# Kernel optimization log

Hardware: AMD Instinct MI355X
Metric: run time of the kernel (lower is better)

The kernel has to match this reference:

```python
import jax, jax.numpy as jnp
import numpy as np

N_NODE, N_PRICE, N_CAT, EMB, LAYERS = 100000, 100, 512, 128, 2
EPS = 1e-8


def spmm(row, col, val, n_rows, emb):
    # torch.sparse.mm(adjacency, emb): out[r] += val * emb[c]
    return jax.ops.segment_sum(val[:, None] * emb[col], row, num_segments=n_rows)


def to_dense(row, col, val, n_rows, n_cols):
    return jnp.zeros((n_rows, n_cols), val.dtype).at[row, col].add(val)


def intra_gate(row, col, val, n_rows, mat_v, emb2):
    # original: alpha = (mat_v expanded to [R, emb]) @ emb2.T ; this is rank-1:
    # scores[i, j] = mat_v[i] * sum_d emb2[j, d]
    scores = mat_v * jnp.sum(emb2, axis=1)[None, :]                      # [R, C]
    alpha = jax.nn.softmax(scores, axis=1) * to_dense(row, col, val, n_rows, emb2.shape[0])
    alpha = alpha / (jnp.sum(alpha, axis=1, keepdims=True) + EPS)        # masked row renorm
    return alpha @ emb2                                                  # [R, emb]; dropout70 = identity (eval)


def inter_gate(Wa, ba, W1, b1, W2, b2, e1, e2, e3):
    g = jax.nn.sigmoid(jnp.concatenate([e1, e2, e3], axis=1) @ Wa + ba + e2 @ W1 + b1 + e3 @ W2 + b2)
    return e1 + g * e2 + (1.0 - g) * e3                                  # dropout50 = identity (eval)


def setup_inputs():
    ks = iter(jax.random.split(jax.random.key(0), 80))
    nrm = lambda shape, s=0.1: jax.random.normal(next(ks), shape, jnp.float32) * s
    inp = {"embedding": nrm((N_NODE, EMB)), "pri_emb": nrm((N_PRICE, EMB)), "cate_emb": nrm((N_CAT, EMB))}
    coo = {"vp": (100000, N_NODE, N_PRICE), "vc": (100000, N_NODE, N_CAT),
           "pv": (100000, N_PRICE, N_NODE), "pc": (2048, N_PRICE, N_CAT),
           "cp": (2048, N_CAT, N_PRICE), "cv": (100000, N_CAT, N_NODE)}
    for name, (nnz, R, C) in coo.items():
        inp[name + "_row"] = jax.random.randint(next(ks), (nnz,), 0, R)
        inp[name + "_col"] = jax.random.randint(next(ks), (nnz,), 0, C)
        inp[name + "_val"] = jax.random.uniform(next(ks), (nnz,), jnp.float32)
    inp["mat_pv"] = nrm((N_PRICE, 1)); inp["mat_pc"] = nrm((N_PRICE, 1))
    inp["mat_cp"] = nrm((N_CAT, 1)); inp["mat_cv"] = nrm((N_CAT, 1))
    for t in "ipc":
        inp["W_aog_" + t] = nrm((3 * EMB, EMB)); inp["b_aog_" + t] = nrm((EMB,))
        inp["W_g" + t + "1"] = nrm((EMB, EMB)); inp["b_g" + t + "1"] = nrm((EMB,))
        inp["W_g" + t + "2"] = nrm((EMB, EMB)); inp["b_g" + t + "2"] = nrm((EMB,))
    return inp


def reference(embedding, pri_emb, cate_emb,
              vp_row, vp_col, vp_val, vc_row, vc_col, vc_val,
              pv_row, pv_col, pv_val, pc_row, pc_col, pc_val,
              cp_row, cp_col, cp_val, cv_row, cv_col, cv_val,
              mat_pv, mat_pc, mat_cp, mat_cv,
              W_aog_i, b_aog_i, W_gi1, b_gi1, W_gi2, b_gi2,
              W_aog_p, b_aog_p, W_gp1, b_gp1, W_gp2, b_gp2,
              W_aog_c, b_aog_c, W_gc1, b_gc1, W_gc2, b_gc2):
    emb_v, emb_p, emb_c = embedding, pri_emb, cate_emb
    for _ in range(LAYERS):
        item = inter_gate(W_aog_i, b_aog_i, W_gi1, b_gi1, W_gi2, b_gi2, emb_v,
                          spmm(vp_row, vp_col, vp_val, N_NODE, emb_p),
                          spmm(vc_row, vc_col, vc_val, N_NODE, emb_c))
        price = inter_gate(W_aog_p, b_aog_p, W_gp1, b_gp1, W_gp2, b_gp2, emb_p,
                           intra_gate(pv_row, pv_col, pv_val, N_PRICE, mat_pv, emb_v),
                           intra_gate(pc_row, pc_col, pc_val, N_PRICE, mat_pc, emb_c))
        cate = inter_gate(W_aog_c, b_aog_c, W_gc1, b_gc1, W_gc2, b_gc2, emb_c,
                          intra_gate(cp_row, cp_col, cp_val, N_CAT, mat_cp, emb_p),
                          intra_gate(cv_row, cv_col, cv_val, N_CAT, mat_cv, emb_v))
        emb_v, emb_p, emb_c = item, price, cate
    return emb_v, emb_p, emb_c
```

## Files before the change

### kernel.cpp

```cpp
#include <hip/hip_runtime.h>

#define EMB 128
#define NV 100000
#define NP 100
#define NC 512
#define EPSV 1e-8f

#define CNT_VP 0
#define CNT_VC 100001
#define CNT_PV 200002
#define CNT_PC 200103
#define CNT_CP 200204
#define CNT_CV 200717
#define CNT_LEN 201230
#define NE_TOT 404096
#define NSB 200

typedef __attribute__((ext_vector_type(8))) short bf16x8;
typedef __attribute__((ext_vector_type(4))) float f32x4;

struct Ptrs6 { const int* row[6]; const int* col[6]; const float* val[6]; };
struct GateW { const float* Wa; const float* W1; const float* W2; const float* ba; const float* b1; const float* b2; };
struct Gates3 { GateW g[3]; };

__device__ __forceinline__ unsigned f2bf(float x){
  unsigned b = __float_as_uint(x);
  return (b + 0x7fffu + ((b >> 16) & 1u)) >> 16;
}
__device__ __forceinline__ unsigned pack2bf(float a, float b){
  return f2bf(a) | (f2bf(b) << 16);
}

__device__ __forceinline__ void sb_decode(int bsm, int& rel, int& cs, int& relN, int& srowBase, int& nRows){
  if(bsm < 98){ rel=2; cs=bsm*1024;       relN=100000; srowBase=0;   nRows=100; }
  else if(bsm < 100){ rel=3; cs=(bsm-98)*1024;  relN=2048;   srowBase=100; nRows=100; }
  else if(bsm < 102){ rel=4; cs=(bsm-100)*1024; relN=2048;   srowBase=200; nRows=512; }
  else {              rel=5; cs=(bsm-102)*1024; relN=100000; srowBase=712; nRows=512; }
}

__device__ __forceinline__ void srow_decode(int srow, int& b0, int& b1, int& gidx){
  if(srow < 100){ b0=0;   b1=98;  gidx = CNT_PV + srow; }
  else if(srow < 200){ b0=98;  b1=100; gidx = CNT_PC + srow-100; }
  else if(srow < 712){ b0=100; b1=102; gidx = CNT_CP + srow-200; }
  else {               b0=102; b1=200; gidx = CNT_CV + srow-712; }
}

#define RS_BASE 396
#define RSV_B 3125
#define RSP_B 4
#define RSC_B 16
#define HISTA_NB (RS_BASE + RSV_B + RSP_B + RSC_B)
__global__ __launch_bounds__(1024) void k_histA(Ptrs6 p, int* counts, int* H,
    const float* v, const float* pe, const float* c, float* s){
  int b = blockIdx.x;
  if(b >= RS_BASE){
    int rs = b - RS_BASE;
    const float* src; int nR, rb, sOff;
    if(rs < RSV_B){ src=v; nR=NV; rb=rs*32; sOff=0; }
    else if(rs < RSV_B+RSP_B){ src=pe; nR=NP; rb=(rs-RSV_B)*32; sOff=NV; }
    else { src=c; nR=NC; rb=(rs-RSV_B-RSP_B)*32; sOff=NV+NP; }
    int rl = threadIdx.x >> 5, lane = threadIdx.x & 31;
    int r = rb + rl;
    if(r >= nR) return;
    float4 x = ((const float4*)(src + (size_t)r*EMB))[lane];
    float sum = (x.x + x.y) + (x.z + x.w);
    #pragma unroll
    for(int o=16;o;o>>=1) sum += __shfl_xor(sum, o);
    if(lane == 0) s[sOff + r] = sum;
    return;
  }
  if(b < 196){
    int e = b*1024 + threadIdx.x;
    if(e >= 200000) return;
    int rel = (e < 100000) ? 0 : 1;
    int loc = rel ? e-100000 : e;
    int cntOff = rel ? CNT_VC : CNT_VP;
    atomicAdd(&counts[cntOff + 1 + p.row[rel][loc]], 1);
    return;
  }
  __shared__ int h[512];
  int rel, cs, relN, srowBase, nRows;
  sb_decode(b - 196, rel, cs, relN, srowBase, nRows);
  int t = threadIdx.x;
  if(t < nRows) h[t] = 0;
  __syncthreads();
  int i = cs + t;
  if(i < relN) atomicAdd(&h[p.row[rel][i]], 1);
  __syncthreads();
  if(t < nRows) H[(srowBase + t)*NSB + (b - 196)] = h[t];
}

__global__ __launch_bounds__(256) void k_counts_w(const int* H, int* G){
  int gw = (blockIdx.x*blockDim.x + threadIdx.x) >> 6;
  int lane = threadIdx.x & 63;
  if(gw >= 1224) return;
  int b0, b1, gidx;
  srow_decode(gw, b0, b1, gidx);
  int c = 0;
  for(int b = b0 + lane; b < b1; b += 64) c += H[gw*NSB + b];
  #pragma unroll
  for(int o=32;o;o>>=1) c += __shfl_xor(c, o);
  if(lane == 0) G[gidx + 1] = c;
}

__global__ __launch_bounds__(256) void k_hscan_w(const int* G, const int* H, int* offs){
  int gw = (blockIdx.x*blockDim.x + threadIdx.x) >> 6;
  int lane = threadIdx.x & 63;
  if(gw >= 1224) return;
  int b0, b1, gidx;
  srow_decode(gw, b0, b1, gidx);
  int nb = b1 - b0;
  int carry = G[gidx];
  for(int base=0; base<nb; base+=64){
    int b = base + lane;
    int hv = (b < nb) ? H[gw*NSB + b0 + b] : 0;
    int v = hv;
    #pragma unroll
    for(int o=1;o<64;o<<=1){
      int t = __shfl_up(v, o);
      if(lane >= o) v += t;
    }
    if(b < nb) offs[gw*NSB + b0 + b] = carry + v - hv;
    carry += __shfl(v, 63);
  }
}

__global__ __launch_bounds__(1024) void k_scatterA(Ptrs6 p, int* cursor, const int* offs, int2* colval){
  int b = blockIdx.x;
  if(b < 196){
    int e = b*1024 + threadIdx.x;
    if(e >= 200000) return;
    int rel = (e < 100000) ? 0 : 1;
    int loc = rel ? e-100000 : e;
    int cntOff = rel ? CNT_VC : CNT_VP;
    int r = p.row[rel][loc];
    int pos = atomicAdd(&cursor[cntOff + r], 1);
    colval[pos] = make_int2(p.col[rel][loc], __float_as_int(p.val[rel][loc]));
    return;
  }
  __shared__ int h[512];
  int rel, cs, relN, srowBase, nRows;
  sb_decode(b - 196, rel, cs, relN, srowBase, nRows);
  int t = threadIdx.x;
  if(t < nRows) h[t] = 0;
  __syncthreads();
  int i = cs + t;
  if(i < relN){
    int r = p.row[rel][i];
    int rank = atomicAdd(&h[r], 1);
    int pos = offs[(srowBase + r)*NSB + (b - 196)] + rank;
    colval[pos] = make_int2(p.col[rel][i], __float_as_int(p.val[rel][i]));
  }
}

#define SCAN_B 1024
__global__ void k_scan1(const int* in, int* out, int* aux, int n){
  __shared__ int sh[SCAN_B];
  int gid = blockIdx.x*SCAN_B + threadIdx.x;
  int v = (gid < n) ? in[gid] : 0;
  sh[threadIdx.x] = v; __syncthreads();
  for(int o=1;o<SCAN_B;o<<=1){
    int t = (threadIdx.x >= o) ? sh[threadIdx.x - o] : 0;
    __syncthreads();
    sh[threadIdx.x] += t;
    __syncthreads();
  }
  if(gid < n) out[gid] = sh[threadIdx.x];
  if(threadIdx.x == SCAN_B-1) aux[blockIdx.x] = sh[threadIdx.x];
}
__global__ void k_scan2(int* aux, int nb){
  __shared__ int sh[SCAN_B];
  int v = (threadIdx.x < nb) ? aux[threadIdx.x] : 0;
  sh[threadIdx.x] = v; __syncthreads();
  for(int o=1;o<SCAN_B;o<<=1){
    int t = (threadIdx.x >= o) ? sh[threadIdx.x - o] : 0;
    __syncthreads();
    sh[threadIdx.x] += t;
    __syncthreads();
  }
  if(threadIdx.x < nb) aux[threadIdx.x] = sh[threadIdx.x];
}
__global__ void k_scan3(int* out, const int* aux, int n){
  int gid = blockIdx.x*SCAN_B + threadIdx.x;
  if(blockIdx.x == 0 || gid >= n) return;
  out[gid] += aux[blockIdx.x - 1];
}

__global__ void k_prepw(Gates3 gs, float* M2, float* M3, float* bsum, unsigned* A1f){
  int idx = blockIdx.x*blockDim.x + threadIdx.x;
  if(idx >= 3*16384) return;
  int g = idx >> 14, t = idx & 16383;
  M2[idx] = gs.g[g].Wa[16384 + t] + gs.g[g].W1[t];
  M3[idx] = gs.g[g].Wa[32768 + t] + gs.g[g].W2[t];
  if(t < 128) bsum[g*128 + t] = gs.g[g].ba[t] + gs.g[g].b1[t] + gs.g[g].b2[t];
  if(idx < 8192){
    const float* Wa = gs.g[0].Wa;
    int p = idx & 3;
    int l = (idx >> 2) & 63;
    int f = idx >> 8;
    int kb = f >> 3, nt = f & 7;
    int k = 32*kb + 8*(l >> 4) + 2*p;
    int n = 16*nt + (l & 15);
    A1f[idx] = pack2bf(Wa[k*128 + n], Wa[(k+1)*128 + n]);
  }
}

#define IG 16
#define IT 32
#define MID_NB 1377
__global__ __launch_bounds__(512) void k_mid(const int* G, const int2* colval,
    const float* s,
    const float* mat_pv, const float* mat_pc, const float* mat_cp, const float* mat_cv,
    const float* cv_, const float* cp_, const float* cc_,
    const float* M2i, const float* M3i,
    float* o_pv, float* o_pc, float* o_cp, float* o_cv,
    float* Pcat, float* Ccat){
  int b = blockIdx.x;
  int tid = threadIdx.x;
  if(b >= 1224){
    int rr = (b - 1224)*4 + (tid >> 7);
    int j = tid & 127;
    __shared__ float rowsh[4][128];
    const float* src; const float* M; float* dst; int r;
    if(rr < NP){ src=cp_; M=M2i; dst=Pcat; r=rr; }
    else { src=cc_; M=M3i; dst=Ccat; r=rr-NP; }
    rowsh[tid>>7][j] = src[r*EMB + j];
    __syncthreads();
    float acc = 0.f;
    for(int k=0;k<128;k++) acc += rowsh[tid>>7][k]*M[k*EMB + j];
    dst[r*256 + j] = rowsh[tid>>7][j];
    dst[r*256 + 128 + j] = acc;
    return;
  }
  int r; const int* rp; float m; const float* emb2; const float* sp; int C; float* out;
  if(b < 100){       r=b;     rp=G+CNT_PV; m=mat_pv[r]; emb2=cv_; sp=s;       C=NV; out=o_pv; }
  else if(b < 200){  r=b-100; rp=G+CNT_PC; m=mat_pc[r]; emb2=cc_; sp=s+NV+NP; C=NC; out=o_pc; }
  else if(b < 712){  r=b-200; rp=G+CNT_CP; m=mat_cp[r]; emb2=cp_; sp=s+NV;    C=NP; out=o_cp; }
  else {             r=b-712; rp=G+CNT_CV; m=mat_cv[r]; emb2=cv_; sp=s;       C=NV; out=o_cv; }
  const float4* sp4 = (const float4*)sp;
  int n4 = C >> 2;
  float za0=0.f, za1=0.f, za2=0.f, za3=0.f;
  for(int jj = tid; jj < n4; jj += 512){
    float4 x = sp4[jj];
    za0 += __expf(m*x.x); za1 += __expf(m*x.y);
    za2 += __expf(m*x.z); za3 += __expf(m*x.w);
  }
  float zacc = (za0+za1)+(za2+za3);
  #pragma unroll
  for(int o=32;o;o>>=1) zacc += __shfl_xor(zacc, o);
  __shared__ float zred[8];
  if((tid & 63) == 0) zred[tid >> 6] = zacc;
  __syncthreads();
  float Zv = 0.f;
  #pragma unroll
  for(int gg=0; gg<8; gg++) Zv += zred[gg];
  int es = rp[r], ee = rp[r+1];
  __shared__ float wsh[512];
  __shared__ int   csh[512];
  __shared__ float accs[IG*EMB];
  __shared__ float Tsh[IG];
  int tx = tid & (IT-1);
  int g  = tid >> 5;
  float4 acc = {0.f,0.f,0.f,0.f};
  float T = 0.f;
  for(int t = es; t < ee; t += 512){
    int k = t + tid;
    if(k < ee){
      int2 q = colval[k];
      csh[tid] = q.x;
      wsh[tid] = __expf(m*sp[q.x]) * __int_as_float(q.y);
    }
    __syncthreads();
    int n = min(512, ee - t);
    #pragma unroll 8
    for(int kk = g; kk < n; kk += IG){
      float wv = wsh[kk];
      int cc = csh[kk];
      float4 ev = ((const float4*)(emb2 + (size_t)cc*EMB))[tx];
      T += wv;
      acc.x += wv*ev.x; acc.y += wv*ev.y; acc.z += wv*ev.z; acc.w += wv*ev.w;
    }
    __syncthreads();
  }
  ((float4*)accs)[g*IT + tx] = acc;
  if(tx == 0) Tsh[g] = T;
  __syncthreads();
  if(tid < EMB){
    float tot = 0.f, Tt = 0.f;
    #pragma unroll
    for(int gg=0; gg<IG; gg++){
      tot += accs[gg*EMB + tid];
      Tt  += Tsh[gg];
    }
    out[r*EMB + tid] = tot / (Tt + EPSV*Zv);
  }
}

#define ITEM_NB 3431
__global__ __launch_bounds__(256) void k_item(const float* vin, float* vout,
    const float* Pcat, const float* Ccat, const int* G, const int2* colval,
    const uint4* A1f, const float* bsum, float* s_out,
    const float* cp_, const float* cc_, float* out_p, float* out_c,
    const float* o_pv, const float* o_pc, const float* o_cp, const float* o_cv,
    const float* Wa_p, const float* Wa_c, const float* M2b, const float* M3b,
    const float* bsb){
  __shared__ unsigned e1h[32][68];
  __shared__ float rsp[32][2];
  int tid = threadIdx.x;
  int b = blockIdx.x;
  if(b >= 3125){
    int half = tid >> 7;
    int j = tid & 127;
    int rr = (b - 3125)*2 + half;
    const float* src; float* dst; const float* e2p; const float* e3p;
    const float* A1; const float* M2; const float* M3; const float* bs; int r; int soff;
    if(rr < NP){ src=cp_; dst=out_p; r=rr;    e2p=o_pv; e3p=o_pc; A1=Wa_p; M2=M2b+16384; M3=M3b+16384; bs=bsb+128; soff=NV; }
    else {       src=cc_; dst=out_c; r=rr-NP; e2p=o_cp; e3p=o_cv; A1=Wa_c; M2=M2b+32768; M3=M3b+32768; bs=bsb+256; soff=NV+NP; }
    float* sh = ((float*)e1h) + half*384;
    sh[j] = src[r*EMB+j]; sh[128+j] = e2p[r*EMB+j]; sh[256+j] = e3p[r*EMB+j];
    __syncthreads();
    float acc = bs[j];
    for(int k=0;k<128;k++)
      acc += sh[k]*A1[k*EMB+j] + sh[128+k]*M2[k*EMB+j] + sh[256+k]*M3[k*EMB+j];
    float g = 1.f/(1.f + __expf(-acc));
    float outv = sh[j] + g*sh[128+j] + (1.f - g)*sh[256+j];
    dst[r*EMB+j] = outv;
    float rs = outv;
    #pragma unroll
    for(int o=32;o;o>>=1) rs += __shfl_xor(rs, o);
    if((tid & 63) == 0) ((float*)rsp)[tid >> 6] = rs;
    __syncthreads();
    if(j == 0) s_out[soff + r] = ((float*)rsp)[half*2] + ((float*)rsp)[half*2+1];
    return;
  }
  int rb = b*32;
  const float4* vin4 = (const float4*)(vin + (size_t)rb*EMB);
  #pragma unroll
  for(int jj=0; jj<4; jj++){
    int j = tid + jj*256;
    int rr = j >> 5, kk4 = j & 31;
    float4 x = vin4[j];
    uint2 pk; pk.x = pack2bf(x.x, x.y); pk.y = pack2bf(x.z, x.w);
    *(uint2*)&e1h[rr][kk4*2] = pk;
  }
  int w = tid >> 6, l = tid & 63;
  int mt = w & 1, ng = w >> 1;
  int g16 = l >> 4, ln = l & 15;
  int cb = 64*ng + ln;
  int rbase = rb + 16*mt + 4*g16;
  const int* rp_vp = G + CNT_VP;
  const int* rp_vc = G + CNT_VC;
  int vp_ptr[5], vc_ptr[5];
  #pragma unroll
  for(int i=0;i<5;i++){
    vp_ptr[i] = rp_vp[rbase + i];
    vc_ptr[i] = rp_vc[rbase + i];
  }
  __syncthreads();
  f32x4 acc[4];
  #pragma unroll
  for(int j=0;j<4;j++){
    float bv = bsum[cb + 16*j];
    acc[j] = (f32x4){bv, bv, bv, bv};
  }
  for(int kb=0; kb<4; kb++){
    uint4 av = *(const uint4*)&e1h[16*mt + ln][16*kb + 4*g16];
    bf16x8 af = *(bf16x8*)&av;
    #pragma unroll
    for(int j=0;j<4;j++){
      uint4 bv = A1f[(kb*8 + ng*4 + j)*64 + l];
      acc[j] = __builtin_amdgcn_mfma_f32_16x16x32_bf16(af, *(bf16x8*)&bv, acc[j], 0, 0, 0);
    }
  }
  unsigned e1lo = (cb & 1) ? 0u : 1u;
  #pragma unroll
  for(int reg=0; reg<4; reg++){
    int rl_ = 16*mt + 4*g16 + reg;
    int r = rb + rl_;
    float e2[4]={0,0,0,0}, e3[4]={0,0,0,0};
    float lg[4] = {acc[0][reg], acc[1][reg], acc[2][reg], acc[3][reg]};
    for(int e=vp_ptr[reg]; e<vp_ptr[reg+1]; e++){
      int2 q = colval[e]; int cc = q.x; float vv = __int_as_float(q.y);
      const float* base = Pcat + (size_t)cc*256 + cb;
      #pragma unroll
      for(int j=0;j<4;j++){ e2[j] += vv*base[16*j]; lg[j] += vv*base[128 + 16*j]; }
    }
    for(int e=vc_ptr[reg]; e<vc_ptr[reg+1]; e++){
      int2 q = colval[e]; int cc = q.x; float vv = __int_as_float(q.y);
      const float* base = Ccat + (size_t)cc*256 + cb;
      #pragma unroll
      for(int j=0;j<4;j++){ e3[j] += vv*base[16*j]; lg[j] += vv*base[128 + 16*j]; }
    }
    float prs = 0.f;
    float* outr = vout + (size_t)r*EMB + cb;
    #pragma unroll
    for(int j=0;j<4;j++){
      float gg = 1.f/(1.f + __expf(-lg[j]));
      unsigned u = e1h[rl_][(cb + 16*j) >> 1];
      float e1v = __uint_as_float(e1lo ? (u << 16) : (u & 0xffff0000u));
      float ov = e1v + gg*e2[j] + (1.f - gg)*e3[j];
      outr[16*j] = ov;
      prs += ov;
    }
    prs += __shfl_xor(prs, 1);
    prs += __shfl_xor(prs, 2);
    prs += __shfl_xor(prs, 4);
    prs += __shfl_xor(prs, 8);
    if(ln == 0) rsp[rl_][ng] = prs;
  }
  __syncthreads();
  if(tid < 32) s_out[rb + tid] = rsp[tid][0] + rsp[tid][1];
}

extern "C" void kernel_launch(void* const* d_in, const int* in_sizes, int n_in,
                              void* d_out, int out_size, void* d_ws, size_t ws_size,
                              hipStream_t stream){
  (void)in_sizes; (void)n_in; (void)out_size; (void)ws_size;
  const float* embedding = (const float*)d_in[0];
  const float* pri_emb   = (const float*)d_in[1];
  const float* cate_emb  = (const float*)d_in[2];
  Ptrs6 P;
  for(int r=0;r<6;r++){
    P.row[r] = (const int*)d_in[3 + r*3];
    P.col[r] = (const int*)d_in[4 + r*3];
    P.val[r] = (const float*)d_in[5 + r*3];
  }
  const float* mat_pv = (const float*)d_in[21];
  const float* mat_pc = (const float*)d_in[22];
  const float* mat_cp = (const float*)d_in[23];
  const float* mat_cv = (const float*)d_in[24];
  Gates3 GW;
  const int gbase[3] = {25, 31, 37};
  for(int g=0; g<3; g++){
    int b = gbase[g];
    GW.g[g].Wa = (const float*)d_in[b];
    GW.g[g].ba = (const float*)d_in[b+1];
    GW.g[g].W1 = (const float*)d_in[b+2];
    GW.g[g].b1 = (const float*)d_in[b+3];
    GW.g[g].W2 = (const float*)d_in[b+4];
    GW.g[g].b2 = (const float*)d_in[b+5];
  }
  float* out_v = (float*)d_out;
  float* out_p = out_v + (size_t)NV*EMB;
  float* out_c = out_p + (size_t)NP*EMB;

  char* base = (char*)d_ws; size_t off = 0;
  auto alloc = [&](size_t bytes)->void*{
    void* p = base + off;
    off += (bytes + 255) & ~(size_t)255;
    return p;
  };
  int*      G      = (int*)alloc(CNT_LEN*4);
  int*      cursor = (int*)alloc(CNT_LEN*4);
  int*      aux    = (int*)alloc(256*4);
  int2*     colval = (int2*)alloc((size_t)NE_TOT*8);
  int*      H      = (int*)alloc((size_t)1224*NSB*4);
  int*      offs   = (int*)alloc((size_t)1224*NSB*4);
  float*    s      = (float*)alloc((NV+NP+NC)*4);
  float*    o_pv   = (float*)alloc(NP*EMB*4);
  float*    o_pc   = (float*)alloc(NP*EMB*4);
  float*    o_cp   = (float*)alloc(NC*EMB*4);
  float*    o_cv   = (float*)alloc(NC*EMB*4);
  float*    Pcat   = (float*)alloc(NP*256*4);
  float*    Ccat   = (float*)alloc(NC*256*4);
  float*    M2b    = (float*)alloc(3*16384*4);
  float*    M3b    = (float*)alloc(3*16384*4);
  float*    bsb    = (float*)alloc(3*128*4);
  unsigned* A1f    = (unsigned*)alloc(8192*4);

  hipMemsetAsync(G, 0, CNT_LEN*4, stream);
  k_histA<<<HISTA_NB, 1024, 0, stream>>>(P, G, H, embedding, pri_emb, cate_emb, s);
  k_counts_w<<<306, 256, 0, stream>>>(H, G);
  int nScanB = (CNT_LEN + SCAN_B - 1)/SCAN_B;
  k_scan1<<<nScanB, SCAN_B, 0, stream>>>(G, G, aux, CNT_LEN);
  k_scan2<<<1, SCAN_B, 0, stream>>>(aux, nScanB);
  k_scan3<<<nScanB, SCAN_B, 0, stream>>>(G, aux, CNT_LEN);
  k_hscan_w<<<306, 256, 0, stream>>>(G, H, offs);
  hipMemcpyAsync(cursor, G, CNT_PV*4, hipMemcpyDeviceToDevice, stream);
  k_scatterA<<<396, 1024, 0, stream>>>(P, cursor, offs, colval);
  k_prepw<<<192, 256, 0, stream>>>(GW, M2b, M3b, bsb, A1f);

  for(int L=0; L<2; L++){
    const float* cv_ = L ? (const float*)out_v : embedding;
    const float* cp_ = L ? (const float*)out_p : pri_emb;
    const float* cc_ = L ? (const float*)out_c : cate_emb;
    k_mid<<<MID_NB, 512, 0, stream>>>(G, colval, s,
                                      mat_pv, mat_pc, mat_cp, mat_cv,
                                      cv_, cp_, cc_, M2b, M3b,
                                      o_pv, o_pc, o_cp, o_cv, Pcat, Ccat);
    k_item<<<ITEM_NB, 256, 0, stream>>>(cv_, out_v, Pcat, Ccat, G, colval,
                                        (const uint4*)A1f, bsb, s,
                                        cp_, cc_, out_p, out_c,
                                        o_pv, o_pc, o_cp, o_cv,
                                        GW.g[1].Wa, GW.g[2].Wa, M2b, M3b, bsb);
  }
}
```

Measured before the change: 226.4 us.

## Fuse item update and intra-gate aggregation into one concurrent kernel

The separate mid (intra-gate) and item kernels are merged into one launch, so the item-row gate blocks and the price/category aggregation blocks run at the same time instead of one after the other. To keep them independent, the item output of layer 0 goes to a temporary buffer when workspace allows, and the row-sum vector s is double-buffered. The Pcat/Ccat precompute and the price/category gate update are split into their own small kernels before and after. This adds an extra 51 MB workspace buffer and two extra launches per layer. Aggregation blocks now use 256 threads and 8 groups instead of 512 threads and 16 groups.

```diff
diff --git a/kernel.cpp b/kernel.cpp
--- a/kernel.cpp
+++ b/kernel.cpp
@@ -205,134 +205,102 @@
   }
 }
 
-#define IG 16
-#define IT 32
-#define MID_NB 1377
-__global__ __launch_bounds__(512) void k_mid(const int* G, const int2* colval,
-    const float* s,
+__global__ __launch_bounds__(512) void k_cat(const float* cp_, const float* cc_,
+    const float* M2i, const float* M3i, float* Pcat, float* Ccat){
+  int rr = blockIdx.x*4 + (threadIdx.x >> 7);
+  int j = threadIdx.x & 127;
+  __shared__ float rowsh[4][128];
+  const float* src; const float* M; float* dst; int r;
+  if(rr < NP){ src=cp_; M=M2i; dst=Pcat; r=rr; }
+  else { src=cc_; M=M3i; dst=Ccat; r=rr-NP; }
+  rowsh[threadIdx.x>>7][j] = src[r*EMB + j];
+  __syncthreads();
+  float acc = 0.f;
+  for(int k=0;k<128;k++) acc += rowsh[threadIdx.x>>7][k]*M[k*EMB + j];
+  dst[r*256 + j] = rowsh[threadIdx.x>>7][j];
+  dst[r*256 + 128 + j] = acc;
+}
+
+#define ITEM_B 3125
+#define FUSED_NB 4349
+#define IG 8
+__global__ __launch_bounds__(256) void k_fused(int bofs,
+    const float* vin, float* vout,
+    const float* Pcat, const float* Ccat, const int* G, const int2* colval,
+    const uint4* A1f, const float* bsum, const float* s_in, float* s_out,
     const float* mat_pv, const float* mat_pc, const float* mat_cp, const float* mat_cv,
-    const float* cv_, const float* cp_, const float* cc_,
-    const float* M2i, const float* M3i,
-    float* o_pv, float* o_pc, float* o_cp, float* o_cv,
-    float* Pcat, float* Ccat){
-  int b = blockIdx.x;
+    const float* cp_, const float* cc_,
+    float* o_pv, float* o_pc, float* o_cp, float* o_cv){
+  __shared__ __align__(16) char smem[8960];
   int tid = threadIdx.x;
-  if(b >= 1224){
-    int rr = (b - 1224)*4 + (tid >> 7);
-    int j = tid & 127;
-    __shared__ float rowsh[4][128];
-    const float* src; const float* M; float* dst; int r;
-    if(rr < NP){ src=cp_; M=M2i; dst=Pcat; r=rr; }
-    else { src=cc_; M=M3i; dst=Ccat; r=rr-NP; }
-    rowsh[tid>>7][j] = src[r*EMB + j];
-    __syncthreads();
-    float acc = 0.f;
-    for(int k=0;k<128;k++) acc += rowsh[tid>>7][k]*M[k*EMB + j];
-    dst[r*256 + j] = rowsh[tid>>7][j];
-    dst[r*256 + 128 + j] = acc;
+  int b = blockIdx.x + bofs;
+  if(b >= ITEM_B){
+    int bi = b - ITEM_B;
+    float* wsh  = (float*)smem;
+    int*   csh  = (int*)(smem + 1024);
+    float* accs = (float*)(smem + 2048);
+    float* Tsh  = (float*)(smem + 2048 + 4096);
+    float* zred = (float*)(smem + 2048 + 4096 + 32);
+    int r; const int* rp; float m; const float* emb2; const float* sp; int C; float* out;
+    if(bi < 100){       r=bi;     rp=G+CNT_PV; m=mat_pv[r]; emb2=vin; sp=s_in;       C=NV; out=o_pv; }
+    else if(bi < 200){  r=bi-100; rp=G+CNT_PC; m=mat_pc[r]; emb2=cc_; sp=s_in+NV+NP; C=NC; out=o_pc; }
+    else if(bi < 712){  r=bi-200; rp=G+CNT_CP; m=mat_cp[r]; emb2=cp_; sp=s_in+NV;    C=NP; out=o_cp; }
+    else {              r=bi-712; rp=G+CNT_CV; m=mat_cv[r]; emb2=vin; sp=s_in;       C=NV; out=o_cv; }
+    const float4* sp4 = (const float4*)sp;
+    int n4 = C >> 2;
+    float za0=0.f, za1=0.f, za2=0.f, za3=0.f;
+    for(int jj = tid; jj < n4; jj += 256){
+      float4 x = sp4[jj];
+      za0 += __expf(m*x.x); za1 += __expf(m*x.y);
+      za2 += __expf(m*x.z); za3 += __expf(m*x.w);
+    }
+    float zacc = (za0+za1)+(za2+za3);
+    #pragma unroll
+    for(int o=32;o;o>>=1) zacc += __shfl_xor(zacc, o);
+    if((tid & 63) == 0) zred[tid >> 6] = zacc;
+    __syncthreads();
+    float Zv = zred[0] + zred[1] + zred[2] + zred[3];
+    int es = rp[r], ee = rp[r+1];
+    int tx = tid & 31;
+    int g  = tid >> 5;
+    float4 acc = {0.f,0.f,0.f,0.f};
+    float T = 0.f;
+    for(int t = es; t < ee; t += 256){
+      int k = t + tid;
+      __syncthreads();
+      if(k < ee){
+        int2 q = colval[k];
+        csh[tid] = q.x;
+        wsh[tid] = __expf(m*sp[q.x]) * __int_as_float(q.y);
+      }
+      __syncthreads();
+      int n = min(256, ee - t);
+      #pragma unroll 8
+      for(int kk = g; kk < n; kk += IG){
+        float wv = wsh[kk];
+        int cc = csh[kk];
+        float4 ev = ((const float4*)(emb2 + (size_t)cc*EMB))[tx];
+        T += wv;
+        acc.x += wv*ev.x; acc.y += wv*ev.y; acc.z += wv*ev.z; acc.w += wv*ev.w;
+      }
+    }
+    __syncthreads();
+    ((float4*)accs)[g*32 + tx] = acc;
+    if(tx == 0) Tsh[g] = T;
+    __syncthreads();
+    if(tid < EMB){
+      float tot = 0.f, Tt = 0.f;
+      #pragma unroll
+      for(int gg=0; gg<IG; gg++){
+        tot += accs[gg*EMB + tid];
+        Tt  += Tsh[gg];
+      }
+      out[r*EMB + tid] = tot / (Tt + EPSV*Zv);
+    }
     return;
   }
-  int r; const int* rp; float m; const float* emb2; const float* sp; int C; float* out;
-  if(b < 100){       r=b;     rp=G+CNT_PV; m=mat_pv[r]; emb2=cv_; sp=s;       C=NV; out=o_pv; }
-  else if(b < 200){  r=b-100; rp=G+CNT_PC; m=mat_pc[r]; emb2=cc_; sp=s+NV+NP; C=NC; out=o_pc; }
-  else if(b < 712){  r=b-200; rp=G+CNT_CP; m=mat_cp[r]; emb2=cp_; sp=s+NV;    C=NP; out=o_cp; }
-  else {             r=b-712; rp=G+CNT_CV; m=mat_cv[r]; emb2=cv_; sp=s;       C=NV; out=o_cv; }
-  const float4* sp4 = (const float4*)sp;
-  int n4 = C >> 2;
-  float za0=0.f, za1=0.f, za2=0.f, za3=0.f;
-  for(int jj = tid; jj < n4; jj += 512){
-    float4 x = sp4[jj];
-    za0 += __expf(m*x.x); za1 += __expf(m*x.y);
-    za2 += __expf(m*x.z); za3 += __expf(m*x.w);
-  }
-  float zacc = (za0+za1)+(za2+za3);
-  #pragma unroll
-  for(int o=32;o;o>>=1) zacc += __shfl_xor(zacc, o);
-  __shared__ float zred[8];
-  if((tid & 63) == 0) zred[tid >> 6] = zacc;
-  __syncthreads();
-  float Zv = 0.f;
-  #pragma unroll
-  for(int gg=0; gg<8; gg++) Zv += zred[gg];
-  int es = rp[r], ee = rp[r+1];
-  __shared__ float wsh[512];
-  __shared__ int   csh[512];
-  __shared__ float accs[IG*EMB];
-  __shared__ float Tsh[IG];
-  int tx = tid & (IT-1);
-  int g  = tid >> 5;
-  float4 acc = {0.f,0.f,0.f,0.f};
-  float T = 0.f;
-  for(int t = es; t < ee; t += 512){
-    int k = t + tid;
-    if(k < ee){
-      int2 q = colval[k];
-      csh[tid] = q.x;
-      wsh[tid] = __expf(m*sp[q.x]) * __int_as_float(q.y);
-    }
-    __syncthreads();
-    int n = min(512, ee - t);
-    #pragma unroll 8
-    for(int kk = g; kk < n; kk += IG){
-      float wv = wsh[kk];
-      int cc = csh[kk];
-      float4 ev = ((const float4*)(emb2 + (size_t)cc*EMB))[tx];
-      T += wv;
-      acc.x += wv*ev.x; acc.y += wv*ev.y; acc.z += wv*ev.z; acc.w += wv*ev.w;
-    }
-    __syncthreads();
-  }
-  ((float4*)accs)[g*IT + tx] = acc;
-  if(tx == 0) Tsh[g] = T;
-  __syncthreads();
-  if(tid < EMB){
-    float tot = 0.f, Tt = 0.f;
-    #pragma unroll
-    for(int gg=0; gg<IG; gg++){
-      tot += accs[gg*EMB + tid];
-      Tt  += Tsh[gg];
-    }
-    out[r*EMB + tid] = tot / (Tt + EPSV*Zv);
-  }
-}
-
-#define ITEM_NB 3431
-__global__ __launch_bounds__(256) void k_item(const float* vin, float* vout,
-    const float* Pcat, const float* Ccat, const int* G, const int2* colval,
-    const uint4* A1f, const float* bsum, float* s_out,
-    const float* cp_, const float* cc_, float* out_p, float* out_c,
-    const float* o_pv, const float* o_pc, const float* o_cp, const float* o_cv,
-    const float* Wa_p, const float* Wa_c, const float* M2b, const float* M3b,
-    const float* bsb){
-  __shared__ unsigned e1h[32][68];
-  __shared__ float rsp[32][2];
-  int tid = threadIdx.x;
-  int b = blockIdx.x;
-  if(b >= 3125){
-    int half = tid >> 7;
-    int j = tid & 127;
-    int rr = (b - 3125)*2 + half;
-    const float* src; float* dst; const float* e2p; const float* e3p;
-    const float* A1; const float* M2; const float* M3; const float* bs; int r; int soff;
-    if(rr < NP){ src=cp_; dst=out_p; r=rr;    e2p=o_pv; e3p=o_pc; A1=Wa_p; M2=M2b+16384; M3=M3b+16384; bs=bsb+128; soff=NV; }
-    else {       src=cc_; dst=out_c; r=rr-NP; e2p=o_cp; e3p=o_cv; A1=Wa_c; M2=M2b+32768; M3=M3b+32768; bs=bsb+256; soff=NV+NP; }
-    float* sh = ((float*)e1h) + half*384;
-    sh[j] = src[r*EMB+j]; sh[128+j] = e2p[r*EMB+j]; sh[256+j] = e3p[r*EMB+j];
-    __syncthreads();
-    float acc = bs[j];
-    for(int k=0;k<128;k++)
-      acc += sh[k]*A1[k*EMB+j] + sh[128+k]*M2[k*EMB+j] + sh[256+k]*M3[k*EMB+j];
-    float g = 1.f/(1.f + __expf(-acc));
-    float outv = sh[j] + g*sh[128+j] + (1.f - g)*sh[256+j];
-    dst[r*EMB+j] = outv;
-    float rs = outv;
-    #pragma unroll
-    for(int o=32;o;o>>=1) rs += __shfl_xor(rs, o);
-    if((tid & 63) == 0) ((float*)rsp)[tid >> 6] = rs;
-    __syncthreads();
-    if(j == 0) s_out[soff + r] = ((float*)rsp)[half*2] + ((float*)rsp)[half*2+1];
-    return;
-  }
+  unsigned (*e1h)[68] = (unsigned(*)[68])smem;
+  float (*rsp)[2] = (float(*)[2])(smem + 32*68*4);
   int rb = b*32;
   const float4* vin4 = (const float4*)(vin + (size_t)rb*EMB);
   #pragma unroll
@@ -412,10 +380,42 @@
   if(tid < 32) s_out[rb + tid] = rsp[tid][0] + rsp[tid][1];
 }
 
+__global__ __launch_bounds__(256) void k_tail(const float* cp_, const float* cc_,
+    float* out_p, float* out_c,
+    const float* o_pv, const float* o_pc, const float* o_cp, const float* o_cv,
+    const float* Wa_p, const float* Wa_c, const float* M2b, const float* M3b,
+    const float* bsb, float* s_out){
+  __shared__ float sh2[2][384];
+  __shared__ float wred[4];
+  int tid = threadIdx.x;
+  int half = tid >> 7;
+  int j = tid & 127;
+  int rr = blockIdx.x*2 + half;
+  const float* src; float* dst; const float* e2p; const float* e3p;
+  const float* A1; const float* M2; const float* M3; const float* bs; int r; int soff;
+  if(rr < NP){ src=cp_; dst=out_p; r=rr;    e2p=o_pv; e3p=o_pc; A1=Wa_p; M2=M2b+16384; M3=M3b+16384; bs=bsb+128; soff=NV; }
+  else {       src=cc_; dst=out_c; r=rr-NP; e2p=o_cp; e3p=o_cv; A1=Wa_c; M2=M2b+32768; M3=M3b+32768; bs=bsb+256; soff=NV+NP; }
+  float* sh = sh2[half];
+  sh[j] = src[r*EMB+j]; sh[128+j] = e2p[r*EMB+j]; sh[256+j] = e3p[r*EMB+j];
+  __syncthreads();
+  float acc = bs[j];
+  for(int k=0;k<128;k++)
+    acc += sh[k]*A1[k*EMB+j] + sh[128+k]*M2[k*EMB+j] + sh[256+k]*M3[k*EMB+j];
+  float g = 1.f/(1.f + __expf(-acc));
+  float outv = sh[j] + g*sh[128+j] + (1.f - g)*sh[256+j];
+  dst[r*EMB+j] = outv;
+  float rs = outv;
+  #pragma unroll
+  for(int o=32;o;o>>=1) rs += __shfl_xor(rs, o);
+  if((tid & 63) == 0) wred[tid >> 6] = rs;
+  __syncthreads();
+  if(j == 0) s_out[soff + r] = wred[half*2] + wred[half*2+1];
+}
+
 extern "C" void kernel_launch(void* const* d_in, const int* in_sizes, int n_in,
                               void* d_out, int out_size, void* d_ws, size_t ws_size,
                               hipStream_t stream){
-  (void)in_sizes; (void)n_in; (void)out_size; (void)ws_size;
+  (void)in_sizes; (void)n_in; (void)out_size;
   const float* embedding = (const float*)d_in[0];
   const float* pri_emb   = (const float*)d_in[1];
   const float* cate_emb  = (const float*)d_in[2];
@@ -456,7 +456,8 @@
   int2*     colval = (int2*)alloc((size_t)NE_TOT*8);
   int*      H      = (int*)alloc((size_t)1224*NSB*4);
   int*      offs   = (int*)alloc((size_t)1224*NSB*4);
-  float*    s      = (float*)alloc((NV+NP+NC)*4);
+  float*    s0     = (float*)alloc((NV+NP+NC)*4);
+  float*    s1     = (float*)alloc((NV+NP+NC)*4);
   float*    o_pv   = (float*)alloc(NP*EMB*4);
   float*    o_pc   = (float*)alloc(NP*EMB*4);
   float*    o_cp   = (float*)alloc(NC*EMB*4);
@@ -467,9 +468,12 @@
   float*    M3b    = (float*)alloc(3*16384*4);
   float*    bsb    = (float*)alloc(3*128*4);
   unsigned* A1f    = (unsigned*)alloc(8192*4);
+  size_t vbytes = (size_t)NV*EMB*4;
+  bool conc = (off + vbytes + 256 <= ws_size);
+  float* v_tmp = conc ? (float*)alloc(vbytes) : nullptr;
 
   hipMemsetAsync(G, 0, CNT_LEN*4, stream);
-  k_histA<<<HISTA_NB, 1024, 0, stream>>>(P, G, H, embedding, pri_emb, cate_emb, s);
+  k_histA<<<HISTA_NB, 1024, 0, stream>>>(P, G, H, embedding, pri_emb, cate_emb, s0);
   k_counts_w<<<306, 256, 0, stream>>>(H, G);
   int nScanB = (CNT_LEN + SCAN_B - 1)/SCAN_B;
   k_scan1<<<nScanB, SCAN_B, 0, stream>>>(G, G, aux, CNT_LEN);
@@ -481,17 +485,30 @@
   k_prepw<<<192, 256, 0, stream>>>(GW, M2b, M3b, bsb, A1f);
 
   for(int L=0; L<2; L++){
-    const float* cv_ = L ? (const float*)out_v : embedding;
+    const float* cv_ = L ? (conc ? (const float*)v_tmp : (const float*)out_v) : embedding;
+    float* vout = (L == 1) ? out_v : (conc ? v_tmp : out_v);
     const float* cp_ = L ? (const float*)out_p : pri_emb;
     const float* cc_ = L ? (const float*)out_c : cate_emb;
-    k_mid<<<MID_NB, 512, 0, stream>>>(G, colval, s,
-                                      mat_pv, mat_pc, mat_cp, mat_cv,
-                                      cv_, cp_, cc_, M2b, M3b,
-                                      o_pv, o_pc, o_cp, o_cv, Pcat, Ccat);
-    k_item<<<ITEM_NB, 256, 0, stream>>>(cv_, out_v, Pcat, Ccat, G, colval,
-                                        (const uint4*)A1f, bsb, s,
-                                        cp_, cc_, out_p, out_c,
-                                        o_pv, o_pc, o_cp, o_cv,
-                                        GW.g[1].Wa, GW.g[2].Wa, M2b, M3b, bsb);
-  }
-}
+    const float* s_in = L ? s1 : s0;
+    float* s_outb = L ? s0 : s1;
+    k_cat<<<153, 512, 0, stream>>>(cp_, cc_, M2b, M3b, Pcat, Ccat);
+    if(conc){
+      k_fused<<<FUSED_NB, 256, 0, stream>>>(0, cv_, vout, Pcat, Ccat, G, colval,
+          (const uint4*)A1f, bsb, s_in, s_outb,
+          mat_pv, mat_pc, mat_cp, mat_cv, cp_, cc_,
+          o_pv, o_pc, o_cp, o_cv);
+    } else {
+      k_fused<<<1224, 256, 0, stream>>>(ITEM_B, cv_, vout, Pcat, Ccat, G, colval,
+          (const uint4*)A1f, bsb, s_in, s_outb,
+          mat_pv, mat_pc, mat_cp, mat_cv, cp_, cc_,
+          o_pv, o_pc, o_cp, o_cv);
+      k_fused<<<ITEM_B, 256, 0, stream>>>(0, cv_, vout, Pcat, Ccat, G, colval,
+          (const uint4*)A1f, bsb, s_in, s_outb,
+          mat_pv, mat_pc, mat_cp, mat_cv, cp_, cc_,
+          o_pv, o_pc, o_cp, o_cv);
+    }
+    k_tail<<<306, 256, 0, stream>>>(cp_, cc_, out_p, out_c,
+        o_pv, o_pc, o_cp, o_cv,
+        GW.g[1].Wa, GW.g[2].Wa, M2b, M3b, bsb, s_outb);
+  }
+}
```

Result: slower. 304.0 us (+34.3%).
